# Kernel optimization log

Hardware: AMD Instinct MI355X
Metric: run time of the kernel (lower is better)

Reference implementation:

```python
import jax, jax.numpy as jnp
import numpy as np

DIM = 768
B, N = 16, 1024
EPS_LN = 1e-5

def _layernorm(x, gamma, beta):
    mu = jnp.mean(x, axis=-1, keepdims=True)
    var = jnp.mean((x - mu) ** 2, axis=-1, keepdims=True)
    return (x - mu) * jax.lax.rsqrt(var + EPS_LN) * gamma + beta

def _gelu(x):
    return jax.nn.gelu(x, approximate=False)

def setup_inputs() -> dict:
    key = jax.random.key(0)
    ks = jax.random.split(key, 10)
    d = DIM
    s1 = 1.0 / np.sqrt(2 * d)
    s = 1.0 / np.sqrt(d)
    return {
        "x": jax.random.normal(ks[0], (B, N, d), dtype=jnp.float32),
        "gamma": jnp.ones((d,), jnp.float32),
        "beta": jnp.zeros((d,), jnp.float32),
        "w1": jax.random.normal(ks[1], (2 * d, d), jnp.float32) * s1,
        "b1": jnp.zeros((d,), jnp.float32),
        "w2": jax.random.normal(ks[2], (d, d), jnp.float32) * s,
        "b2": jnp.zeros((d,), jnp.float32),
        "w3": jax.random.normal(ks[3], (d, d), jnp.float32) * s,
        "b3": jnp.zeros((d,), jnp.float32),
        "w4": jax.random.normal(ks[4], (d, d), jnp.float32) * s,
        "b4": jnp.zeros((d,), jnp.float32),
    }

def reference(x, gamma, beta, w1, b1, w2, b2, w3, b3, w4, b4):
    # x: [B, N, D]
    avg_x = jnp.mean(x, axis=1)                      # [B, D]
    A = avg_x[:, None, :] * jax.nn.sigmoid(_layernorm(x, gamma, beta))  # [B, N, D]
    # batched pairwise Euclidean distance among tokens (replaces python loop)
    sq = jnp.sum(A * A, axis=-1)                     # [B, N]
    d2 = sq[:, :, None] + sq[:, None, :] - 2.0 * jnp.einsum('bnd,bmd->bnm', A, A)
    dist = jnp.sqrt(jnp.clip(d2, 1e-12))             # [B, N, N]
    m = jnp.max(dist, axis=-1)                       # [B, N]
    m_x = x + m[..., None]                           # [B, N, D]
    cat = jnp.concatenate([A, m_x], axis=-1)         # [B, N, 2D]
    m1 = _gelu(cat @ w1 + b1)                        # layer1
    W = _gelu(m1 @ w2 + b2)                          # layer2
    Wdyn = x * W
    l3 = _gelu((m1 * Wdyn) @ w3 + b3)                # layer3
    out = _gelu((x * l3) @ w4 + b4)                  # layer4
    return out.astype(jnp.float32)
```

## Files before the change

kernel.cpp:

```cpp
#include <hip/hip_runtime.h>
#include <hip/hip_fp16.h>
#include <math.h>

#define DIM 768
#define NTOK 1024
#define NBATCH 16
#define BNR (NBATCH * NTOK)

typedef _Float16 f16x8 __attribute__((ext_vector_type(8)));
typedef float f32x4 __attribute__((ext_vector_type(4)));

__device__ __forceinline__ void gl2lds16(const void* g, void* l) {
    __builtin_amdgcn_global_load_lds(
        (const __attribute__((address_space(1))) void*)g,
        (__attribute__((address_space(3))) void*)l, 16, 0, 0);
}

__device__ __forceinline__ float gelu_fast(float z) {
    const float s = z * 0.70710678118654752f;
    const float ax = fabsf(s);
    const float t = __builtin_amdgcn_rcpf(1.0f + 0.3275911f * ax);
    const float poly = t * (0.254829592f + t * (-0.284496736f +
                       t * (1.421413741f + t * (-1.453152027f + t * 1.061405429f))));
    const float e = __expf(-ax * ax);
    float erfv = 1.0f - poly * e;
    erfv = copysignf(erfv, s);
    return 0.5f * z * (1.0f + erfv);
}

__device__ __forceinline__ float block_sum(float v, float* sbuf) {
    #pragma unroll
    for (int o = 32; o > 0; o >>= 1) v += __shfl_down(v, o, 64);
    const int lane = threadIdx.x & 63, w = threadIdx.x >> 6;
    if (lane == 0) sbuf[w] = v;
    __syncthreads();
    const float r = sbuf[0] + sbuf[1] + sbuf[2] + sbuf[3];
    __syncthreads();
    return r;
}

__global__ __launch_bounds__(256) void avg_kernel(const float* __restrict__ x,
                                                  float* __restrict__ avgx) {
    const int d = blockIdx.x * 256 + threadIdx.x;
    const int b = blockIdx.y;
    const int n0 = blockIdx.z * 128;
    const float* xp = x + (size_t)b * NTOK * DIM + (size_t)n0 * DIM + d;
    float s = 0.0f;
    for (int n = 0; n < 128; ++n) s += xp[(size_t)n * DIM];
    atomicAdd(&avgx[b * DIM + d], s * (1.0f / NTOK));
}

__global__ __launch_bounds__(256) void ln_sig_kernel(
    const float* __restrict__ x, const float* __restrict__ gamma,
    const float* __restrict__ beta, const float* __restrict__ avgx,
    __half* __restrict__ Ah, float* __restrict__ sq)
{
    __shared__ float sbuf[4];
    const int row = blockIdx.x;
    const int b = row >> 10;
    const int tid = threadIdx.x;
    const float* xr = x + (size_t)row * DIM;
    float v[3];
    #pragma unroll
    for (int i = 0; i < 3; ++i) v[i] = xr[tid + 256 * i];
    const float mu = block_sum(v[0] + v[1] + v[2], sbuf) * (1.0f / DIM);
    float ss = 0.0f;
    #pragma unroll
    for (int i = 0; i < 3; ++i) { const float d = v[i] - mu; ss += d * d; }
    const float var = block_sum(ss, sbuf) * (1.0f / DIM);
    const float rstd = rsqrtf(var + 1e-5f);
    const float* ag = avgx + b * DIM;
    float qs = 0.0f;
    #pragma unroll
    for (int i = 0; i < 3; ++i) {
        const int d = tid + 256 * i;
        const float ln = (v[i] - mu) * rstd * gamma[d] + beta[d];
        const float sg = 1.0f / (1.0f + expf(-ln));
        const float a = ag[d] * sg;
        const __half h = __float2half(a);
        const float ar = __half2float(h);
        Ah[(size_t)row * DIM + d] = h;
        qs += ar * ar;
    }
    const float tot = block_sum(qs, sbuf);
    if (tid == 0) sq[row] = tot;
}

__device__ __forceinline__ void wconv_body(const float* __restrict__ w,
                                           __half* __restrict__ wT, int K, int N,
                                           int bx, int by)
{
    __shared__ float t[64][65];
    const int k0 = by * 64, n0 = bx * 64;
    const int tid = threadIdx.x;
    const int r = tid >> 4, c4 = (tid & 15) * 4;
    #pragma unroll
    for (int p = 0; p < 4; ++p) {
        const int rr = p * 16 + r;
        const float4 v = *(const float4*)&w[(size_t)(k0 + rr) * N + n0 + c4];
        t[rr][c4] = v.x; t[rr][c4 + 1] = v.y; t[rr][c4 + 2] = v.z; t[rr][c4 + 3] = v.w;
    }
    __syncthreads();
    #pragma unroll
    for (int p = 0; p < 4; ++p) {
        const int nn = p * 16 + r;
        ushort4 pk;
        pk.x = __half_as_ushort(__float2half(t[c4 + 0][nn]));
        pk.y = __half_as_ushort(__float2half(t[c4 + 1][nn]));
        pk.z = __half_as_ushort(__float2half(t[c4 + 2][nn]));
        pk.w = __half_as_ushort(__float2half(t[c4 + 3][nn]));
        *(ushort4*)&wT[(size_t)(n0 + nn) * K + k0 + c4] = pk;
    }
}

__global__ __launch_bounds__(256) void wconv(const float* __restrict__ w,
                                             __half* __restrict__ wT, int K, int N)
{
    wconv_body(w, wT, K, N, blockIdx.x, blockIdx.y);
}

__global__ __launch_bounds__(256) void wconv3(const float* __restrict__ w2,
                                              const float* __restrict__ w3,
                                              const float* __restrict__ w4,
                                              __half* __restrict__ t2,
                                              __half* __restrict__ t3,
                                              __half* __restrict__ t4)
{
    const float* w = (blockIdx.z == 0) ? w2 : (blockIdx.z == 1) ? w3 : w4;
    __half* wT = (blockIdx.z == 0) ? t2 : (blockIdx.z == 1) ? t3 : t4;
    wconv_body(w, wT, 768, 768, blockIdx.x, blockIdx.y);
}

__global__ __launch_bounds__(256) void xm_kernel(const float* __restrict__ x,
                                                 const float* __restrict__ m,
                                                 __half* __restrict__ xmH) {
    const int row = blockIdx.x;
    const float mv = m[row];
    #pragma unroll
    for (int i = 0; i < 3; ++i) {
        const int d = threadIdx.x + i * 256;
        xmH[(size_t)row * DIM + d] = __float2half(x[(size_t)row * DIM + d] + mv);
    }
}

template<int K, bool CAT, int EPI>
__global__ __launch_bounds__(256, 4) void gemm16(
    const __half* __restrict__ A0, const __half* __restrict__ A1,
    const __half* __restrict__ BT, const float* __restrict__ bias,
    const float* __restrict__ xin, const __half* __restrict__ m1h,
    __half* __restrict__ outH, float* __restrict__ outF)
{
    __shared__ _Float16 As[2][128 * 32];
    __shared__ _Float16 Bs[2][128 * 32];
    const int tid = threadIdx.x;
    const int w = tid >> 6, lane = tid & 63;
    const int wu = __builtin_amdgcn_readfirstlane(w);
    const int wr = w >> 1, wc = w & 1;
    const int R0 = blockIdx.x * 128, J0 = blockIdx.y * 128;
    constexpr int rs = CAT ? DIM : K;
    const int srow = lane >> 2;
    const int sk8 = (((lane & 3) ^ ((lane >> 3) & 3))) * 8;
    const int fx = ((lane >> 4) ^ ((lane >> 1) & 3)) * 8;
    constexpr int NT = K / 32;

    f32x4 acc[4][4];
    #pragma unroll
    for (int mt = 0; mt < 4; ++mt)
        #pragma unroll
        for (int nt = 0; nt < 4; ++nt) {
            f32x4 z = {0.0f, 0.0f, 0.0f, 0.0f};
            acc[mt][nt] = z;
        }

    auto stage = [&](int buf, int k0) {
        const __half* Ab = (CAT && k0 >= DIM) ? (A1 + (k0 - DIM)) : (A0 + k0);
        #pragma unroll
        for (int i = 0; i < 2; ++i) {
            const int rbase = i * 64 + w * 16;
            const int rbu = i * 64 + wu * 16;
            gl2lds16(Ab + (size_t)(R0 + rbase + srow) * rs + sk8, &As[buf][rbu * 32]);
            gl2lds16(BT + (size_t)(J0 + rbase + srow) * K + k0 + sk8, &Bs[buf][rbu * 32]);
        }
    };

    stage(0, 0);
    __syncthreads();
    #pragma unroll 2
    for (int kt = 0; kt < NT; ++kt) {
        const int cur = kt & 1;
        if (kt + 1 < NT) stage(cur ^ 1, (kt + 1) * 32);
        f16x8 af[4], bf[4];
        #pragma unroll
        for (int mt = 0; mt < 4; ++mt)
            af[mt] = *(const f16x8*)&As[cur][(wr * 64 + mt * 16 + (lane & 15)) * 32 + fx];
        #pragma unroll
        for (int nt = 0; nt < 4; ++nt)
            bf[nt] = *(const f16x8*)&Bs[cur][(wc * 64 + nt * 16 + (lane & 15)) * 32 + fx];
        #pragma unroll
        for (int mt = 0; mt < 4; ++mt)
            #pragma unroll
            for (int nt = 0; nt < 4; ++nt)
                acc[mt][nt] = __builtin_amdgcn_mfma_f32_16x16x32_f16(af[mt], bf[nt], acc[mt][nt], 0, 0, 0);
        __syncthreads();
    }

    #pragma unroll
    for (int mt = 0; mt < 4; ++mt) {
        #pragma unroll
        for (int nt = 0; nt < 4; ++nt) {
            const int col = J0 + wc * 64 + nt * 16 + (lane & 15);
            const float bv = bias[col];
            #pragma unroll
            for (int r = 0; r < 4; ++r) {
                const int row = R0 + wr * 64 + mt * 16 + (lane >> 4) * 4 + r;
                const size_t off = (size_t)row * DIM + col;
                const float g = gelu_fast(acc[mt][nt][r] + bv);
                if (EPI == 0) {
                    outH[off] = __float2half(g);
                } else if (EPI == 1) {
                    outH[off] = __float2half(__half2float(m1h[off]) * xin[off] * g);
                } else if (EPI == 2) {
                    outH[off] = __float2half(xin[off] * g);
                } else {
                    outF[off] = g;
                }
            }
        }
    }
}

__global__ __launch_bounds__(256, 4) void dist16(const __half* __restrict__ Ah,
                                                 const float* __restrict__ sq,
                                                 float* __restrict__ m)
{
    __shared__ _Float16 As[2][128 * 32];
    __shared__ _Float16 Bs[2][128 * 32];
    const int tid = threadIdx.x;
    const int w = tid >> 6, lane = tid & 63;
    const int wu = __builtin_amdgcn_readfirstlane(w);
    const int wr = w >> 1, wc = w & 1;
    const int base = blockIdx.x * NTOK;
    int t = blockIdx.y, ty = 0;
    while (t >= 8 - ty) { t -= 8 - ty; ++ty; }
    const int tz = ty + t;
    const int I0 = ty * 128, J0 = tz * 128;
    const int srow = lane >> 2;
    const int sk8 = (((lane & 3) ^ ((lane >> 3) & 3))) * 8;
    const int fx = ((lane >> 4) ^ ((lane >> 1) & 3)) * 8;
    constexpr int NT = DIM / 32;

    f32x4 acc[4][4];
    #pragma unroll
    for (int mt = 0; mt < 4; ++mt)
        #pragma unroll
        for (int nt = 0; nt < 4; ++nt) {
            f32x4 z = {0.0f, 0.0f, 0.0f, 0.0f};
            acc[mt][nt] = z;
        }

    auto stage = [&](int buf, int k0) {
        #pragma unroll
        for (int i = 0; i < 2; ++i) {
            const int rbase = i * 64 + w * 16;
            const int rbu = i * 64 + wu * 16;
            gl2lds16(Ah + (size_t)(base + I0 + rbase + srow) * DIM + k0 + sk8, &As[buf][rbu * 32]);
            gl2lds16(Ah + (size_t)(base + J0 + rbase + srow) * DIM + k0 + sk8, &Bs[buf][rbu * 32]);
        }
    };

    stage(0, 0);
    __syncthreads();
    #pragma unroll 2
    for (int kt = 0; kt < NT; ++kt) {
        const int cur = kt & 1;
        if (kt + 1 < NT) stage(cur ^ 1, (kt + 1) * 32);
        f16x8 af[4], bf[4];
        #pragma unroll
        for (int mt = 0; mt < 4; ++mt)
            af[mt] = *(const f16x8*)&As[cur][(wr * 64 + mt * 16 + (lane & 15)) * 32 + fx];
        #pragma unroll
        for (int nt = 0; nt < 4; ++nt)
            bf[nt] = *(const f16x8*)&Bs[cur][(wc * 64 + nt * 16 + (lane & 15)) * 32 + fx];
        #pragma unroll
        for (int mt = 0; mt < 4; ++mt)
            #pragma unroll
            for (int nt = 0; nt < 4; ++nt)
                acc[mt][nt] = __builtin_amdgcn_mfma_f32_16x16x32_f16(af[mt], bf[nt], acc[mt][nt], 0, 0, 0);
        __syncthreads();
    }

    float sqiA[4][4];
    #pragma unroll
    for (int mt = 0; mt < 4; ++mt)
        #pragma unroll
        for (int r = 0; r < 4; ++r)
            sqiA[mt][r] = sq[base + I0 + wr * 64 + mt * 16 + (lane >> 4) * 4 + r];
    float sqjA[4];
    #pragma unroll
    for (int nt = 0; nt < 4; ++nt)
        sqjA[nt] = sq[base + J0 + wc * 64 + nt * 16 + (lane & 15)];

    #pragma unroll
    for (int mt = 0; mt < 4; ++mt) {
        float vmax[4] = {-1e30f, -1e30f, -1e30f, -1e30f};
        #pragma unroll
        for (int nt = 0; nt < 4; ++nt)
            #pragma unroll
            for (int r = 0; r < 4; ++r)
                vmax[r] = fmaxf(vmax[r], sqiA[mt][r] + sqjA[nt] - 2.0f * acc[mt][nt][r]);
        #pragma unroll
        for (int r = 0; r < 4; ++r) {
            float v = vmax[r];
            v = fmaxf(v, __shfl_xor(v, 1, 64));
            v = fmaxf(v, __shfl_xor(v, 2, 64));
            v = fmaxf(v, __shfl_xor(v, 4, 64));
            v = fmaxf(v, __shfl_xor(v, 8, 64));
            if ((lane & 15) == 0) {
                const float d = sqrtf(fmaxf(v, 1e-12f));
                atomicMax((unsigned int*)&m[base + I0 + wr * 64 + mt * 16 + (lane >> 4) * 4 + r],
                          __float_as_uint(d));
            }
        }
    }

    if (I0 != J0) {
        #pragma unroll
        for (int nt = 0; nt < 4; ++nt) {
            float cm = -1e30f;
            #pragma unroll
            for (int mt = 0; mt < 4; ++mt)
                #pragma unroll
                for (int r = 0; r < 4; ++r)
                    cm = fmaxf(cm, sqiA[mt][r] + sqjA[nt] - 2.0f * acc[mt][nt][r]);
            cm = fmaxf(cm, __shfl_xor(cm, 16, 64));
            cm = fmaxf(cm, __shfl_xor(cm, 32, 64));
            if ((lane >> 4) == 0) {
                const float d = sqrtf(fmaxf(cm, 1e-12f));
                atomicMax((unsigned int*)&m[base + J0 + wc * 64 + nt * 16 + (lane & 15)],
                          __float_as_uint(d));
            }
        }
    }
}

extern "C" void kernel_launch(void* const* d_in, const int* in_sizes, int n_in,
                              void* d_out, int out_size, void* d_ws, size_t ws_size,
                              hipStream_t stream)
{
    const float* x     = (const float*)d_in[0];
    const float* gamma = (const float*)d_in[1];
    const float* beta  = (const float*)d_in[2];
    const float* w1    = (const float*)d_in[3];
    const float* b1    = (const float*)d_in[4];
    const float* w2    = (const float*)d_in[5];
    const float* b2    = (const float*)d_in[6];
    const float* w3    = (const float*)d_in[7];
    const float* b3    = (const float*)d_in[8];
    const float* w4    = (const float*)d_in[9];
    const float* b4    = (const float*)d_in[10];
    float* out = (float*)d_out;
    float* ws  = (float*)d_ws;

    float* avgx = ws;
    float* mbuf = ws + 12288;
    float* sq   = mbuf + 16384;
    __half* w1T = (__half*)(sq + 16384);
    __half* w2T = w1T + (size_t)1536 * 768;
    __half* w3T = w2T + (size_t)768 * 768;
    __half* w4T = w3T + (size_t)768 * 768;
    __half* P0  = w4T + (size_t)768 * 768;
    __half* P1  = P0 + (size_t)BNR * DIM;
    __half* Ah  = (__half*)d_out;
    __half* xmH = Ah + (size_t)BNR * DIM;

    hipMemsetAsync(ws, 0, (12288 + 16384) * sizeof(float), stream);
    wconv<<<dim3(12, 24), 256, 0, stream>>>(w1, w1T, 1536, 768);
    wconv3<<<dim3(12, 12, 3), 256, 0, stream>>>(w2, w3, w4, w2T, w3T, w4T);
    avg_kernel<<<dim3(3, NBATCH, 8), 256, 0, stream>>>(x, avgx);
    ln_sig_kernel<<<BNR, 256, 0, stream>>>(x, gamma, beta, avgx, Ah, sq);
    dist16<<<dim3(NBATCH, 36), 256, 0, stream>>>(Ah, sq, mbuf);
    xm_kernel<<<BNR, 256, 0, stream>>>(x, mbuf, xmH);
    gemm16<1536, true, 0><<<dim3(128, 6), 256, 0, stream>>>(
        Ah, xmH, w1T, b1, nullptr, nullptr, P0, nullptr);
    gemm16<768, false, 1><<<dim3(128, 6), 256, 0, stream>>>(
        P0, nullptr, w2T, b2, x, P0, P1, nullptr);
    gemm16<768, false, 2><<<dim3(128, 6), 256, 0, stream>>>(
        P1, nullptr, w3T, b3, x, nullptr, P0, nullptr);
    gemm16<768, false, 3><<<dim3(128, 6), 256, 0, stream>>>(
        P0, nullptr, w4T, b4, x, nullptr, nullptr, out);
}
```

Baseline: 334.2 us.

## Fold row-max broadcast into layer1 epilogue via w1 column sums, drop xm kernel

Uses linearity: (x + m)·w1b = x·w1b + m·colsum(w1b), so the fp16 x copy is written once in the LN kernel and the per-row max term is added in the layer1 GEMM epilogue as m[row]*s1[col]. This removes the separate xm_kernel pass over the activations and lets the layer1 A operand be produced before the distance kernel finishes. The LN/sigmoid kernel is also rewritten to process one row per wavefront with float4 loads and shuffle-only reductions, dropping shared-memory block syncs. It adds a small column-sum kernel over w1 and changes rounding, since m is no longer quantised to fp16 together with x.

```diff
diff --git a/kernel.cpp b/kernel.cpp
--- a/kernel.cpp
+++ b/kernel.cpp
@@ -28,17 +28,6 @@
     return 0.5f * z * (1.0f + erfv);
 }
 
-__device__ __forceinline__ float block_sum(float v, float* sbuf) {
-    #pragma unroll
-    for (int o = 32; o > 0; o >>= 1) v += __shfl_down(v, o, 64);
-    const int lane = threadIdx.x & 63, w = threadIdx.x >> 6;
-    if (lane == 0) sbuf[w] = v;
-    __syncthreads();
-    const float r = sbuf[0] + sbuf[1] + sbuf[2] + sbuf[3];
-    __syncthreads();
-    return r;
-}
-
 __global__ __launch_bounds__(256) void avg_kernel(const float* __restrict__ x,
                                                   float* __restrict__ avgx) {
     const int d = blockIdx.x * 256 + threadIdx.x;
@@ -50,40 +39,75 @@
     atomicAdd(&avgx[b * DIM + d], s * (1.0f / NTOK));
 }
 
+__global__ __launch_bounds__(256) void colsum_w1b(const float* __restrict__ w1,
+                                                  float* __restrict__ s1) {
+    const int col = blockIdx.x * 256 + threadIdx.x;
+    const int r0 = 768 + blockIdx.y * 64;
+    float s = 0.0f;
+    #pragma unroll 8
+    for (int r = 0; r < 64; ++r) s += w1[(size_t)(r0 + r) * 768 + col];
+    atomicAdd(&s1[col], s);
+}
+
 __global__ __launch_bounds__(256) void ln_sig_kernel(
     const float* __restrict__ x, const float* __restrict__ gamma,
     const float* __restrict__ beta, const float* __restrict__ avgx,
-    __half* __restrict__ Ah, float* __restrict__ sq)
-{
-    __shared__ float sbuf[4];
-    const int row = blockIdx.x;
+    __half* __restrict__ Ah, __half* __restrict__ xh, float* __restrict__ sq)
+{
+    const int wv = threadIdx.x >> 6, lane = threadIdx.x & 63;
+    const int row = blockIdx.x * 4 + wv;
     const int b = row >> 10;
-    const int tid = threadIdx.x;
     const float* xr = x + (size_t)row * DIM;
-    float v[3];
-    #pragma unroll
-    for (int i = 0; i < 3; ++i) v[i] = xr[tid + 256 * i];
-    const float mu = block_sum(v[0] + v[1] + v[2], sbuf) * (1.0f / DIM);
+    float4 v[3];
+    #pragma unroll
+    for (int i = 0; i < 3; ++i) v[i] = *(const float4*)&xr[i * 256 + lane * 4];
+    float s = v[0].x + v[0].y + v[0].z + v[0].w
+            + v[1].x + v[1].y + v[1].z + v[1].w
+            + v[2].x + v[2].y + v[2].z + v[2].w;
+    #pragma unroll
+    for (int o = 32; o > 0; o >>= 1) s += __shfl_xor(s, o, 64);
+    const float mu = s * (1.0f / DIM);
     float ss = 0.0f;
     #pragma unroll
-    for (int i = 0; i < 3; ++i) { const float d = v[i] - mu; ss += d * d; }
-    const float var = block_sum(ss, sbuf) * (1.0f / DIM);
-    const float rstd = rsqrtf(var + 1e-5f);
-    const float* ag = avgx + b * DIM;
+    for (int i = 0; i < 3; ++i) {
+        const float dx0 = v[i].x - mu, dx1 = v[i].y - mu, dx2 = v[i].z - mu, dx3 = v[i].w - mu;
+        ss += dx0 * dx0 + dx1 * dx1 + dx2 * dx2 + dx3 * dx3;
+    }
+    #pragma unroll
+    for (int o = 32; o > 0; o >>= 1) ss += __shfl_xor(ss, o, 64);
+    const float rstd = rsqrtf(ss * (1.0f / DIM) + 1e-5f);
     float qs = 0.0f;
     #pragma unroll
     for (int i = 0; i < 3; ++i) {
-        const int d = tid + 256 * i;
-        const float ln = (v[i] - mu) * rstd * gamma[d] + beta[d];
-        const float sg = 1.0f / (1.0f + expf(-ln));
-        const float a = ag[d] * sg;
-        const __half h = __float2half(a);
-        const float ar = __half2float(h);
-        Ah[(size_t)row * DIM + d] = h;
-        qs += ar * ar;
-    }
-    const float tot = block_sum(qs, sbuf);
-    if (tid == 0) sq[row] = tot;
+        const int d0 = i * 256 + lane * 4;
+        const float4 g4 = *(const float4*)&gamma[d0];
+        const float4 b4 = *(const float4*)&beta[d0];
+        const float4 a4 = *(const float4*)&avgx[b * DIM + d0];
+        ushort4 pa, px;
+        const float xv[4] = {v[i].x, v[i].y, v[i].z, v[i].w};
+        const float gv[4] = {g4.x, g4.y, g4.z, g4.w};
+        const float bv[4] = {b4.x, b4.y, b4.z, b4.w};
+        const float av[4] = {a4.x, a4.y, a4.z, a4.w};
+        unsigned short pav[4], pxv[4];
+        #pragma unroll
+        for (int j = 0; j < 4; ++j) {
+            const float ln = (xv[j] - mu) * rstd * gv[j] + bv[j];
+            const float sg = 1.0f / (1.0f + expf(-ln));
+            const float a = av[j] * sg;
+            const __half h = __float2half(a);
+            const float ar = __half2float(h);
+            qs += ar * ar;
+            pav[j] = __half_as_ushort(h);
+            pxv[j] = __half_as_ushort(__float2half(xv[j]));
+        }
+        pa.x = pav[0]; pa.y = pav[1]; pa.z = pav[2]; pa.w = pav[3];
+        px.x = pxv[0]; px.y = pxv[1]; px.z = pxv[2]; px.w = pxv[3];
+        *(ushort4*)&Ah[(size_t)row * DIM + d0] = pa;
+        *(ushort4*)&xh[(size_t)row * DIM + d0] = px;
+    }
+    #pragma unroll
+    for (int o = 32; o > 0; o >>= 1) qs += __shfl_xor(qs, o, 64);
+    if (lane == 0) sq[row] = qs;
 }
 
 __device__ __forceinline__ void wconv_body(const float* __restrict__ w,
@@ -131,23 +155,12 @@
     wconv_body(w, wT, 768, 768, blockIdx.x, blockIdx.y);
 }
 
-__global__ __launch_bounds__(256) void xm_kernel(const float* __restrict__ x,
-                                                 const float* __restrict__ m,
-                                                 __half* __restrict__ xmH) {
-    const int row = blockIdx.x;
-    const float mv = m[row];
-    #pragma unroll
-    for (int i = 0; i < 3; ++i) {
-        const int d = threadIdx.x + i * 256;
-        xmH[(size_t)row * DIM + d] = __float2half(x[(size_t)row * DIM + d] + mv);
-    }
-}
-
 template<int K, bool CAT, int EPI>
 __global__ __launch_bounds__(256, 4) void gemm16(
     const __half* __restrict__ A0, const __half* __restrict__ A1,
     const __half* __restrict__ BT, const float* __restrict__ bias,
     const float* __restrict__ xin, const __half* __restrict__ m1h,
+    const float* __restrict__ mv, const float* __restrict__ sv,
     __half* __restrict__ outH, float* __restrict__ outF)
 {
     __shared__ _Float16 As[2][128 * 32];
@@ -206,23 +219,33 @@
 
     #pragma unroll
     for (int mt = 0; mt < 4; ++mt) {
+        float mrow[4];
+        if constexpr (EPI == 0) {
+            #pragma unroll
+            for (int r = 0; r < 4; ++r)
+                mrow[r] = mv[R0 + wr * 64 + mt * 16 + (lane >> 4) * 4 + r];
+        }
         #pragma unroll
         for (int nt = 0; nt < 4; ++nt) {
             const int col = J0 + wc * 64 + nt * 16 + (lane & 15);
             const float bv = bias[col];
+            float s1c = 0.0f;
+            if constexpr (EPI == 0) s1c = sv[col];
             #pragma unroll
             for (int r = 0; r < 4; ++r) {
                 const int row = R0 + wr * 64 + mt * 16 + (lane >> 4) * 4 + r;
                 const size_t off = (size_t)row * DIM + col;
-                const float g = gelu_fast(acc[mt][nt][r] + bv);
                 if (EPI == 0) {
+                    const float g = gelu_fast(acc[mt][nt][r] + bv + mrow[r] * s1c);
                     outH[off] = __float2half(g);
                 } else if (EPI == 1) {
+                    const float g = gelu_fast(acc[mt][nt][r] + bv);
                     outH[off] = __float2half(__half2float(m1h[off]) * xin[off] * g);
                 } else if (EPI == 2) {
+                    const float g = gelu_fast(acc[mt][nt][r] + bv);
                     outH[off] = __float2half(xin[off] * g);
                 } else {
-                    outF[off] = g;
+                    outF[off] = gelu_fast(acc[mt][nt][r] + bv);
                 }
             }
         }
@@ -363,7 +386,8 @@
 
     float* avgx = ws;
     float* mbuf = ws + 12288;
-    float* sq   = mbuf + 16384;
+    float* s1   = mbuf + 16384;
+    float* sq   = s1 + 768;
     __half* w1T = (__half*)(sq + 16384);
     __half* w2T = w1T + (size_t)1536 * 768;
     __half* w3T = w2T + (size_t)768 * 768;
@@ -371,21 +395,21 @@
     __half* P0  = w4T + (size_t)768 * 768;
     __half* P1  = P0 + (size_t)BNR * DIM;
     __half* Ah  = (__half*)d_out;
-    __half* xmH = Ah + (size_t)BNR * DIM;
-
-    hipMemsetAsync(ws, 0, (12288 + 16384) * sizeof(float), stream);
+    __half* xh  = Ah + (size_t)BNR * DIM;
+
+    hipMemsetAsync(ws, 0, (12288 + 16384 + 768) * sizeof(float), stream);
     wconv<<<dim3(12, 24), 256, 0, stream>>>(w1, w1T, 1536, 768);
     wconv3<<<dim3(12, 12, 3), 256, 0, stream>>>(w2, w3, w4, w2T, w3T, w4T);
+    colsum_w1b<<<dim3(3, 12), 256, 0, stream>>>(w1, s1);
     avg_kernel<<<dim3(3, NBATCH, 8), 256, 0, stream>>>(x, avgx);
-    ln_sig_kernel<<<BNR, 256, 0, stream>>>(x, gamma, beta, avgx, Ah, sq);
+    ln_sig_kernel<<<BNR / 4, 256, 0, stream>>>(x, gamma, beta, avgx, Ah, xh, sq);
     dist16<<<dim3(NBATCH, 36), 256, 0, stream>>>(Ah, sq, mbuf);
-    xm_kernel<<<BNR, 256, 0, stream>>>(x, mbuf, xmH);
     gemm16<1536, true, 0><<<dim3(128, 6), 256, 0, stream>>>(
-        Ah, xmH, w1T, b1, nullptr, nullptr, P0, nullptr);
+        Ah, xh, w1T, b1, nullptr, nullptr, mbuf, s1, P0, nullptr);
     gemm16<768, false, 1><<<dim3(128, 6), 256, 0, stream>>>(
-        P0, nullptr, w2T, b2, x, P0, P1, nullptr);
+        P0, nullptr, w2T, b2, x, P0, nullptr, nullptr, P1, nullptr);
     gemm16<768, false, 2><<<dim3(128, 6), 256, 0, stream>>>(
-        P1, nullptr, w3T, b3, x, nullptr, P0, nullptr);
+        P1, nullptr, w3T, b3, x, nullptr, nullptr, nullptr, P0, nullptr);
     gemm16<768, false, 3><<<dim3(128, 6), 256, 0, stream>>>(
-        P0, nullptr, w4T, b4, x, nullptr, nullptr, out);
-}
+        P0, nullptr, w4T, b4, x, nullptr, nullptr, nullptr, nullptr, out);
+}
```

Measured after the change: 328.7 us. No clear change (-1.6%).
